# Performance work log

Measured on AMD Instinct MI355X. Metric: run time of the kernel, lower is better.

Reference implementation:

```python
import jax, jax.numpy as jnp
import numpy as np

C = 64
N_H = 4
N_WIN = 16
WIN_L = 8   # compressor window length (overlapped)
WIN_S = 4   # compressor stride -> T//4 blocks


def _rms(x, eps=1e-6):
    return x * jax.lax.rsqrt(jnp.mean(x * x, axis=-1, keepdims=True) + eps)


def _rope(x, negate=False):
    # x: (..., L, D); rotate-half RoPE over positions 0..L-1
    L, D = x.shape[-2], x.shape[-1]
    half = D // 2
    inv_freq = 1.0 / (10000.0 ** (jnp.arange(half, dtype=x.dtype) / half))
    ang = jnp.arange(L, dtype=x.dtype)[:, None] * inv_freq  # (L, half)
    if negate:
        ang = -ang
    cos, sin = jnp.cos(ang), jnp.sin(ang)
    x1, x2 = x[..., :half], x[..., half:]
    return jnp.concatenate([x1 * cos - x2 * sin, x1 * sin + x2 * cos], axis=-1)


def _compress(H, W):
    # overlapped token compressor: windows of WIN_L, stride WIN_S, zero-pad tail
    B, T, d = H.shape
    Tc = T // WIN_S
    Hp = jnp.pad(H, ((0, 0), (0, WIN_L - WIN_S), (0, 0)))
    idx = WIN_S * jnp.arange(Tc)[:, None] + jnp.arange(WIN_L)[None, :]  # (Tc, WIN_L)
    win = Hp[:, idx]                       # (B, Tc, WIN_L, d)
    return win.reshape(B, Tc, WIN_L * d) @ W  # (B, Tc, out)


def setup_inputs() -> dict:
    key = jax.random.key(0)
    ks = jax.random.split(key, 11)
    B, T, d = 2, 2048, 256

    def w(k, shape, fan):
        return jax.random.normal(k, shape, jnp.float32) / np.float32(np.sqrt(fan))

    H = jax.random.normal(ks[0], (B, T, d), jnp.float32)
    return {
        'H': H,
        'Wc_comp': w(ks[1], (WIN_L * d, C), WIN_L * d),
        'Wc_idx': w(ks[2], (WIN_L * d, 32), WIN_L * d),
        'W_DQ': w(ks[3], (d, 64), d),
        'W_IUQ': w(ks[4], (64, 4 * 32), 64),
        'W_w': w(ks[5], (64, 4), 64),
        'W_Q': w(ks[6], (d, N_H * C), d),
        'W_KV': w(ks[7], (d, C), d),
        'g_q': jnp.ones((N_H, C), jnp.float32),
        'g_k': jnp.ones((C,), jnp.float32),
        'g_v': jnp.ones((C,), jnp.float32),
        'Wg0': w(ks[8], (2 * C, 64), 2 * C),
        'bg0': jnp.zeros((64,), jnp.float32),
        'Wg1': w(ks[9], (2 * C, 64), 2 * C),
        'bg1': jnp.zeros((64,), jnp.float32),
        'Wout': w(ks[10], (128, d), 128),
        'bout': jnp.zeros((d,), jnp.float32),
    }


def reference(H, Wc_comp, Wc_idx, W_DQ, W_IUQ, W_w, W_Q, W_KV,
              g_q, g_k, g_v, Wg0, bg0, Wg1, bg1, Wout, bout):
    B, T, d = H.shape
    Tc = T // 4
    k_top = min(8, Tc)

    # ---- lightning indexer ----
    H_dc = H @ W_DQ                                   # (B,T,64)
    Q_I = (H_dc @ W_IUQ).reshape(B, T, 4, 32)         # (B,T,4,32)
    W_Iw = (H_dc @ W_w)[..., None]                    # (B,T,4,1)
    K_I = _compress(H, Wc_idx)                        # (B,Tc,32)
    dot = jnp.einsum('bthc,bsc->bths', Q_I, K_I)      # (B,T,4,Tc)
    I_ts = (W_Iw * jax.nn.relu(dot)).sum(axis=2)      # (B,T,Tc)

    t = jnp.arange(T)[:, None]
    s = jnp.arange(Tc)[None, :]
    mask_I = jnp.where(4 * s <= t, 0.0, -jnp.inf)     # (T,Tc) causal over blocks
    _, topk_idx = jax.lax.top_k(I_ts + mask_I, k_top)  # (B,T,k)
    bI = jnp.arange(B)[:, None, None]
    tI = jnp.arange(T)[None, :, None]
    M_comp = jnp.full((B, T, Tc), -jnp.inf).at[bI, tI, topk_idx].set(0.0)

    # ---- compressed + sliding KV ----
    KV = jnp.concatenate([_compress(H, Wc_comp), H @ W_KV], axis=1)  # (B,Tc+T,C)

    Q = (H @ W_Q).reshape(B, T, N_H, C).transpose(0, 2, 1, 3)        # (B,nh,T,C)
    Q = _rms(Q) * g_q[None, :, None, :]
    K = _rms(KV) * g_k
    V = _rms(KV) * g_v
    Q = _rope(Q)
    K = _rope(K)
    V = _rope(V)

    S = jnp.einsum('bhtc,bsc->bhts', Q, K) / np.float32(np.sqrt(C))  # (B,nh,T,Tc+T)

    S_comp = S[..., :Tc] + M_comp[:, None]
    rel = t - jnp.arange(T)[None, :]
    mask_slide = jnp.where((rel >= 0) & (rel < N_WIN), 0.0, -jnp.inf)  # (T,T)
    S_slide = S[..., Tc:] + mask_slide

    P = jax.nn.softmax(jnp.concatenate([S_comp, S_slide], axis=-1), axis=-1)
    O = jnp.einsum('bhts,bsc->bhtc', P, V)            # (B,nh,T,C)
    O = _rope(O, negate=True)

    O0 = O[:, :2].transpose(0, 2, 1, 3).reshape(B, T, 2 * C)
    O1 = O[:, 2:].transpose(0, 2, 1, 3).reshape(B, T, 2 * C)
    p_all = jnp.concatenate([O0 @ Wg0 + bg0, O1 @ Wg1 + bg1], axis=-1)
    return p_all @ Wout + bout
```

## Files before the change

kernel.cpp:

```cpp
#include <hip/hip_runtime.h>
#include <hip/hip_bf16.h>
#include <math.h>

#define T_DIM 2048
#define B_DIM 2
#define D_DIM 256
#define TC 512
#define KV_LEN 2560

typedef __attribute__((ext_vector_type(8))) short bf16x8;
typedef __attribute__((ext_vector_type(4))) float f32x4;
typedef unsigned short ush;

__device__ __forceinline__ float wave_sum64(float v) {
#pragma unroll
    for (int off = 32; off > 0; off >>= 1) v += __shfl_xor(v, off, 64);
    return v;
}

__device__ __forceinline__ float rope_angle(int pos, int j) {
    float inv = powf(10000.0f, -(float)j * (1.0f / 32.0f));
    return (float)pos * inv;
}

__global__ __launch_bounds__(256) void k_prep(
    const float* __restrict__ H, const float* __restrict__ W_Q,
    const float* __restrict__ W_KV, const float* __restrict__ W_DQ,
    const float* __restrict__ Wc_comp, const float* __restrict__ Wc_idx,
    ush* __restrict__ Ap, ush* __restrict__ Ac,
    ush* __restrict__ Bp, ush* __restrict__ Bc)
{
    int gid = blockIdx.x * 256 + threadIdx.x;
    float vals[8];
    ush* dst;
    bool lo_part;

    if (gid < 262144) {
        int tile = gid >> 10;
        int c = (gid >> 6) & 15;
        int l = gid & 63;
        int bt = tile * 16 + (l & 15);
        int kb = (c & 7) * 32 + (l >> 4) * 8;
        const float* src = H + (size_t)bt * 256 + kb;
#pragma unroll
        for (int j = 0; j < 8; ++j) vals[j] = src[j];
        lo_part = (c >= 8);
        dst = Ap + (size_t)gid * 8;
    } else if (gid < 786432) {
        int g = gid - 262144;
        int tile = g >> 13;
        int c = (g >> 6) & 127;
        int l = g & 63;
        int m = tile * 16 + (l & 15);
        int s = m & 511;
        int b = m >> 9;
        int k2b = (c & 63) * 32 + (l >> 4) * 8;
        int r4 = 4 * s + (k2b >> 8);
        int col = k2b & 255;
        if (r4 < T_DIM) {
            const float* src = H + ((size_t)b * T_DIM + r4) * 256 + col;
#pragma unroll
            for (int j = 0; j < 8; ++j) vals[j] = src[j];
        } else {
#pragma unroll
            for (int j = 0; j < 8; ++j) vals[j] = 0.f;
        }
        lo_part = (c >= 64);
        dst = Ac + (size_t)g * 8;
    } else if (gid < 811008) {
        int g = gid - 786432;
        int tile = g >> 10;
        int c = (g >> 6) & 15;
        int l = g & 63;
        int n = tile * 16 + (l & 15);
        int kb = (c & 7) * 32 + (l >> 4) * 8;
#pragma unroll
        for (int j = 0; j < 8; ++j) {
            int k = kb + j;
            float w;
            if (n < 256)      w = W_Q[(size_t)k * 256 + n];
            else if (n < 320) w = W_KV[(size_t)k * 64 + (n - 256)];
            else              w = W_DQ[(size_t)k * 64 + (n - 320)];
            vals[j] = w;
        }
        lo_part = (c >= 8);
        dst = Bp + (size_t)g * 8;
    } else if (gid < 860160) {
        int g = gid - 811008;
        int tile = g >> 13;
        int c = (g >> 6) & 127;
        int l = g & 63;
        int n = tile * 16 + (l & 15);
        int k2b = (c & 63) * 32 + (l >> 4) * 8;
#pragma unroll
        for (int j = 0; j < 8; ++j) {
            int k = k2b + j;
            vals[j] = (n < 64) ? Wc_comp[(size_t)k * 64 + n]
                               : Wc_idx[(size_t)k * 32 + (n - 64)];
        }
        lo_part = (c >= 64);
        dst = Bc + (size_t)g * 8;
    } else {
        return;
    }

    bf16x8 out;
#pragma unroll
    for (int j = 0; j < 8; ++j) {
        float x = vals[j];
        __hip_bfloat16 hb = __float2bfloat16(x);
        if (!lo_part) {
            out[j] = *(short*)&hb;
        } else {
            float hif = __bfloat162float(hb);
            __hip_bfloat16 lb = __float2bfloat16(x - hif);
            out[j] = *(short*)&lb;
        }
    }
    *(bf16x8*)dst = out;
}

__global__ __launch_bounds__(64) void k_mfma(
    const ush* __restrict__ Ap, const ush* __restrict__ Ac,
    const ush* __restrict__ Bp, const ush* __restrict__ Bc,
    float* __restrict__ Pre, float* __restrict__ Prec_part)
{
    int lane = threadIdx.x;
    int mrow = lane & 15;
    int q = lane >> 4;

    f32x4 acc[2][6];
#pragma unroll
    for (int mt = 0; mt < 2; ++mt)
#pragma unroll
        for (int nt = 0; nt < 6; ++nt) acc[mt][nt] = (f32x4){0.f, 0.f, 0.f, 0.f};

    if (blockIdx.x < 512) {
        int p = blockIdx.x;
        int m0 = (p >> 2) * 32;
        int n0 = (p & 3) * 96;
        int at0 = (m0 >> 4) * 16;
        int bt0n = (n0 >> 4) * 16;

        for (int c = 0; c < 8; ++c) {
            bf16x8 ahi[2], alo[2], bhi[6], blo[6];
#pragma unroll
            for (int mt = 0; mt < 2; ++mt) {
                ahi[mt] = *(const bf16x8*)(Ap + (size_t)((at0 + mt * 16) + c) * 512 + lane * 8);
                alo[mt] = *(const bf16x8*)(Ap + (size_t)((at0 + mt * 16) + 8 + c) * 512 + lane * 8);
            }
#pragma unroll
            for (int nt = 0; nt < 6; ++nt) {
                bhi[nt] = *(const bf16x8*)(Bp + (size_t)((bt0n + nt * 16) + c) * 512 + lane * 8);
                blo[nt] = *(const bf16x8*)(Bp + (size_t)((bt0n + nt * 16) + 8 + c) * 512 + lane * 8);
            }
#pragma unroll
            for (int mt = 0; mt < 2; ++mt)
#pragma unroll
                for (int nt = 0; nt < 6; ++nt) {
                    acc[mt][nt] = __builtin_amdgcn_mfma_f32_16x16x32_bf16(ahi[mt], bhi[nt], acc[mt][nt], 0, 0, 0);
                    acc[mt][nt] = __builtin_amdgcn_mfma_f32_16x16x32_bf16(ahi[mt], blo[nt], acc[mt][nt], 0, 0, 0);
                    acc[mt][nt] = __builtin_amdgcn_mfma_f32_16x16x32_bf16(alo[mt], bhi[nt], acc[mt][nt], 0, 0, 0);
                }
        }

#pragma unroll
        for (int mt = 0; mt < 2; ++mt)
#pragma unroll
            for (int nt = 0; nt < 6; ++nt)
#pragma unroll
                for (int reg = 0; reg < 4; ++reg)
                    Pre[(size_t)(m0 + 16 * mt + 4 * q + reg) * 384 + n0 + 16 * nt + mrow] =
                        acc[mt][nt][reg];
    } else {
        int cb = blockIdx.x - 512;
        int m0 = (cb >> 2) * 32;
        int q4 = cb & 3;
        int at0 = (m0 >> 4) * 128;

        for (int cl = 0; cl < 16; ++cl) {
            int c = q4 * 16 + cl;
            bf16x8 ahi[2], alo[2], bhi[6], blo[6];
#pragma unroll
            for (int mt = 0; mt < 2; ++mt) {
                ahi[mt] = *(const bf16x8*)(Ac + (size_t)((at0 + mt * 128) + c) * 512 + lane * 8);
                alo[mt] = *(const bf16x8*)(Ac + (size_t)((at0 + mt * 128) + 64 + c) * 512 + lane * 8);
            }
#pragma unroll
            for (int nt = 0; nt < 6; ++nt) {
                bhi[nt] = *(const bf16x8*)(Bc + (size_t)(nt * 128 + c) * 512 + lane * 8);
                blo[nt] = *(const bf16x8*)(Bc + (size_t)(nt * 128 + 64 + c) * 512 + lane * 8);
            }
#pragma unroll
            for (int mt = 0; mt < 2; ++mt)
#pragma unroll
                for (int nt = 0; nt < 6; ++nt) {
                    acc[mt][nt] = __builtin_amdgcn_mfma_f32_16x16x32_bf16(ahi[mt], bhi[nt], acc[mt][nt], 0, 0, 0);
                    acc[mt][nt] = __builtin_amdgcn_mfma_f32_16x16x32_bf16(ahi[mt], blo[nt], acc[mt][nt], 0, 0, 0);
                    acc[mt][nt] = __builtin_amdgcn_mfma_f32_16x16x32_bf16(alo[mt], bhi[nt], acc[mt][nt], 0, 0, 0);
                }
        }

        float* dst = Prec_part + (size_t)q4 * (1024 * 96);
#pragma unroll
        for (int mt = 0; mt < 2; ++mt)
#pragma unroll
            for (int nt = 0; nt < 6; ++nt)
#pragma unroll
                for (int reg = 0; reg < 4; ++reg)
                    dst[(size_t)(m0 + 16 * mt + 4 * q + reg) * 96 + 16 * nt + mrow] =
                        acc[mt][nt][reg];
    }
}

__global__ __launch_bounds__(256) void k_epi_proj(
    const float* __restrict__ Pre, const float* __restrict__ W_IUQ,
    const float* __restrict__ W_w, const float* __restrict__ g_q,
    const float* __restrict__ g_k, const float* __restrict__ g_v,
    float* __restrict__ QI, float* __restrict__ Wiw, float* __restrict__ Qr,
    float* __restrict__ Kbuf, float* __restrict__ Vbuf)
{
    int tid = threadIdx.x;
    int wv = tid >> 6;
    int lane = tid & 63;
    int bt = blockIdx.x * 4 + wv;
    int b = bt >> 11;
    int t = bt & 2047;

    __shared__ float sWI[8192];
    __shared__ float sWw[256];
    __shared__ float sHdc[4][64];

    for (int i = tid * 4; i < 8192; i += 1024)
        *(float4*)&sWI[i] = *(const float4*)(W_IUQ + i);
    if (tid < 64) ((float4*)sWw)[tid] = ((const float4*)W_w)[tid];

    const float* pr = Pre + (size_t)bt * 384;
    sHdc[wv][lane] = pr[320 + lane];
    __syncthreads();

    int j = lane & 31;
    float s_t, c_t;
    sincosf(rope_angle(t, j), &s_t, &c_t);

#pragma unroll
    for (int r = 0; r < 4; ++r) {
        float qv = pr[r * 64 + lane];
        float ss = wave_sum64(qv * qv);
        float sc = rsqrtf(ss * (1.0f / 64.0f) + 1e-6f);
        float qq = qv * sc * g_q[r * 64 + lane];
        float prt = __shfl_xor(qq, 32, 64);
        float o = (lane < 32) ? fmaf(qq, c_t, -prt * s_t)
                              : fmaf(prt, s_t, qq * c_t);
        Qr[(size_t)bt * 256 + r * 64 + lane] = o;
    }
    {
        float kvv = pr[256 + lane];
        float ss = wave_sum64(kvv * kvv);
        float sc = rsqrtf(ss * (1.0f / 64.0f) + 1e-6f);
        float kk = kvv * sc * g_k[lane];
        float vv = kvv * sc * g_v[lane];
        int pos = TC + t;
        float s_p, c_p;
        sincosf(rope_angle(pos, j), &s_p, &c_p);
        float pk = __shfl_xor(kk, 32, 64);
        float pv = __shfl_xor(vv, 32, 64);
        float ko = (lane < 32) ? fmaf(kk, c_p, -pk * s_p) : fmaf(pk, s_p, kk * c_p);
        float vo = (lane < 32) ? fmaf(vv, c_p, -pv * s_p) : fmaf(pv, s_p, vv * c_p);
        size_t off = ((size_t)b * KV_LEN + pos) * 64 + lane;
        Kbuf[off] = ko;
        Vbuf[off] = vo;
    }
    {
        float a0 = 0.f, a1 = 0.f;
#pragma unroll 8
        for (int jj = 0; jj < 64; ++jj) {
            float hv = sHdc[wv][jj];
            a0 = fmaf(hv, sWI[jj * 128 + lane], a0);
            a1 = fmaf(hv, sWI[jj * 128 + 64 + lane], a1);
        }
        QI[(size_t)bt * 128 + lane] = a0;
        QI[(size_t)bt * 128 + 64 + lane] = a1;
        if (lane < 4) {
            float aw = 0.f;
            for (int jj = 0; jj < 64; ++jj)
                aw = fmaf(sHdc[wv][jj], sWw[jj * 4 + lane], aw);
            Wiw[(size_t)bt * 4 + lane] = aw;
        }
    }
}

__global__ __launch_bounds__(256) void k_epi_comp(
    const float* __restrict__ Prec_part, const float* __restrict__ g_k,
    const float* __restrict__ g_v,
    float* __restrict__ KIbuf, float* __restrict__ Kbuf, float* __restrict__ Vbuf)
{
    int tid = threadIdx.x;
    int wv = tid >> 6;
    int lane = tid & 63;
    int sg = blockIdx.x * 4 + wv;
    int b = sg >> 9;
    int s = sg & 511;

    const float* p0 = Prec_part + (size_t)sg * 96;
    float kvv = p0[lane] + p0[98304 + lane] + p0[2 * 98304 + lane] + p0[3 * 98304 + lane];

    float ss = wave_sum64(kvv * kvv);
    float sc = rsqrtf(ss * (1.0f / 64.0f) + 1e-6f);
    float kk = kvv * sc * g_k[lane];
    float vv = kvv * sc * g_v[lane];
    int j = lane & 31;
    float sa, ca;
    sincosf(rope_angle(s, j), &sa, &ca);
    float pk = __shfl_xor(kk, 32, 64);
    float pv = __shfl_xor(vv, 32, 64);
    float ko = (lane < 32) ? fmaf(kk, ca, -pk * sa) : fmaf(pk, sa, kk * ca);
    float vo = (lane < 32) ? fmaf(vv, ca, -pv * sa) : fmaf(pv, sa, vv * ca);
    size_t off = ((size_t)b * KV_LEN + s) * 64 + lane;
    Kbuf[off] = ko;
    Vbuf[off] = vo;

    if (lane < 32) {
        float a = p0[64 + lane] + p0[98304 + 64 + lane] +
                  p0[2 * 98304 + 64 + lane] + p0[3 * 98304 + 64 + lane];
        KIbuf[((size_t)b * TC + s) * 32 + lane] = a;
    }
}

__global__ __launch_bounds__(256) void k_score_topk(
    const float* __restrict__ QI, const float* __restrict__ Wiw,
    const float* __restrict__ KIbuf, int* __restrict__ topk)
{
    int tid = threadIdx.x;
    int wv = tid >> 6;
    int lane = tid & 63;
    int bt0 = blockIdx.x * 4;
    int bt = bt0 + wv;
    int b = bt >> 11;
    int t = bt & 2047;

    __shared__ float sQ[4][128];
    __shared__ float sw[4][4];
    __shared__ float sKI[64 * 33];

    sQ[wv][lane] = QI[(size_t)bt * 128 + lane];
    sQ[wv][64 + lane] = QI[(size_t)bt * 128 + 64 + lane];
    if (lane < 4) sw[wv][lane] = Wiw[(size_t)bt * 4 + lane];

    const float* KIb = KIbuf + (size_t)b * TC * 32;
    int smax = t >> 2;
    int smax_blk = ((bt0 + 3) & 2047) >> 2;

    float vals[8];
#pragma unroll
    for (int r = 0; r < 8; ++r) vals[r] = -INFINITY;

    for (int r = 0; r < 8; ++r) {
        if (r * 64 > smax_blk) break;
        __syncthreads();
        for (int i = tid; i < 512; i += 256) {
            int row = i >> 3;
            int cseg = (i & 7) * 4;
            float4 v = *(const float4*)(KIb + (size_t)(r * 64 + row) * 32 + cseg);
            float* dst = &sKI[row * 33 + cseg];
            dst[0] = v.x; dst[1] = v.y; dst[2] = v.z; dst[3] = v.w;
        }
        __syncthreads();

        int s = r * 64 + lane;
        if (s <= smax) {
            float dd0 = 0.f, dd1 = 0.f, dd2 = 0.f, dd3 = 0.f;
#pragma unroll
            for (int c = 0; c < 32; ++c) {
                float kv = sKI[lane * 33 + c];
                dd0 = fmaf(sQ[wv][c], kv, dd0);
                dd1 = fmaf(sQ[wv][32 + c], kv, dd1);
                dd2 = fmaf(sQ[wv][64 + c], kv, dd2);
                dd3 = fmaf(sQ[wv][96 + c], kv, dd3);
            }
            vals[r] = sw[wv][0] * fmaxf(dd0, 0.f) + sw[wv][1] * fmaxf(dd1, 0.f) +
                      sw[wv][2] * fmaxf(dd2, 0.f) + sw[wv][3] * fmaxf(dd3, 0.f);
        }
    }

    unsigned consumed = 0u;
    for (int k2 = 0; k2 < 8; ++k2) {
        float bv = -INFINITY;
        int bi = 0x7fffffff;
#pragma unroll
        for (int r = 0; r < 8; ++r) {
            if (!(consumed & (1u << r))) {
                int s = lane + 64 * r;
                float v = vals[r];
                if (v > bv || (v == bv && s < bi)) { bv = v; bi = s; }
            }
        }
#pragma unroll
        for (int off = 1; off < 64; off <<= 1) {
            float ov = __shfl_xor(bv, off, 64);
            int oi = __shfl_xor(bi, off, 64);
            if (ov > bv || (ov == bv && oi < bi)) { bv = ov; bi = oi; }
        }
        if ((bi & 63) == lane) consumed |= 1u << (bi >> 6);
        if (lane == 0) topk[(size_t)bt * 8 + k2] = bi;
    }
}

__global__ __launch_bounds__(1024) void k_attn_out(
    const float* __restrict__ Qr, const float* __restrict__ Kbuf,
    const float* __restrict__ Vbuf, const int* __restrict__ topk,
    const float* __restrict__ Wg0, const float* __restrict__ bg0,
    const float* __restrict__ Wg1, const float* __restrict__ bg1,
    const float* __restrict__ Wout, const float* __restrict__ bout,
    float* __restrict__ out)
{
    int tid = threadIdx.x;
    int lt = tid >> 8;
    int t256 = tid & 255;
    int h = t256 >> 6;
    int lane = tid & 63;
    int bt = blockIdx.x * 4 + lt;
    int b = bt >> 11;
    int t = bt & 2047;

    __shared__ float sKV[4][48 * 65];
    __shared__ float sQ[4][256];
    __shared__ int sPos[4][24];
    __shared__ float sP[4][4][24];
    __shared__ float sO[4][256];
    __shared__ float sPall[4][128];

    sQ[lt][t256] = Qr[(size_t)bt * 256 + t256];
    if (t256 < 8) {
        sPos[lt][t256] = topk[(size_t)bt * 8 + t256];
    } else if (t256 < 24) {
        int rel = t256 - 8;
        int sp = t - rel;
        sPos[lt][t256] = (sp >= 0) ? (TC + sp) : -1;
    }
    __syncthreads();

    for (int i = t256; i < 768; i += 256) {
        int row = i >> 4;
        int seg = (i & 15) << 2;
        int key = (row < 24) ? row : row - 24;
        int pos = sPos[lt][key];
        if (pos >= 0) {
            const float* src = ((row < 24) ? Kbuf : Vbuf) +
                               ((size_t)b * KV_LEN + pos) * 64 + seg;
            float4 v = *(const float4*)src;
            float* dst = &sKV[lt][row * 65 + seg];
            dst[0] = v.x; dst[1] = v.y; dst[2] = v.z; dst[3] = v.w;
        }
    }
    __syncthreads();

    float scv = -INFINITY;
    if (lane < 24) {
        int pos = sPos[lt][lane];
        if (pos >= 0) {
            float dd = 0.f;
#pragma unroll
            for (int c = 0; c < 64; ++c)
                dd = fmaf(sQ[lt][h * 64 + c], sKV[lt][lane * 65 + c], dd);
            scv = dd * 0.125f;
        }
    }
    float m = scv;
#pragma unroll
    for (int off = 1; off < 64; off <<= 1) m = fmaxf(m, __shfl_xor(m, off, 64));
    float p = expf(scv - m);
    if (scv == -INFINITY) p = 0.f;
    float l = p;
#pragma unroll
    for (int off = 1; off < 64; off <<= 1) l += __shfl_xor(l, off, 64);
    p /= l;
    if (lane < 24) sP[lt][h][lane] = p;

    float o = 0.f;
#pragma unroll
    for (int j2 = 0; j2 < 24; ++j2) {
        int pos = sPos[lt][j2];
        if (pos >= 0)
            o = fmaf(sP[lt][h][j2], sKV[lt][(24 + j2) * 65 + lane], o);
    }

    int j = lane & 31;
    float sa, ca;
    sincosf(rope_angle(t, j), &sa, &ca);
    float prt = __shfl_xor(o, 32, 64);
    float oo = (lane < 32) ? fmaf(o, ca, prt * sa) : fmaf(-prt, sa, o * ca);
    sO[lt][h * 64 + lane] = oo;
    __syncthreads();

    if (t256 < 128) {
        float a;
        if (t256 < 64) {
            a = bg0[t256];
            for (int c = 0; c < 128; ++c) a = fmaf(sO[lt][c], Wg0[c * 64 + t256], a);
        } else {
            int i = t256 - 64;
            a = bg1[i];
            for (int c = 0; c < 128; ++c) a = fmaf(sO[lt][128 + c], Wg1[c * 64 + i], a);
        }
        sPall[lt][t256] = a;
    }
    __syncthreads();

    float a = bout[t256];
    for (int i = 0; i < 128; ++i) a = fmaf(sPall[lt][i], Wout[i * 256 + t256], a);
    out[(size_t)bt * 256 + t256] = a;
}

extern "C" void kernel_launch(void* const* d_in, const int* in_sizes, int n_in,
                              void* d_out, int out_size, void* d_ws, size_t ws_size,
                              hipStream_t stream) {
    const float* H       = (const float*)d_in[0];
    const float* Wc_comp = (const float*)d_in[1];
    const float* Wc_idx  = (const float*)d_in[2];
    const float* W_DQ    = (const float*)d_in[3];
    const float* W_IUQ   = (const float*)d_in[4];
    const float* W_w     = (const float*)d_in[5];
    const float* W_Q     = (const float*)d_in[6];
    const float* W_KV    = (const float*)d_in[7];
    const float* g_q     = (const float*)d_in[8];
    const float* g_k     = (const float*)d_in[9];
    const float* g_v     = (const float*)d_in[10];
    const float* Wg0     = (const float*)d_in[11];
    const float* bg0     = (const float*)d_in[12];
    const float* Wg1     = (const float*)d_in[13];
    const float* bg1     = (const float*)d_in[14];
    const float* Wout    = (const float*)d_in[15];
    const float* bout    = (const float*)d_in[16];

    float* ws  = (float*)d_ws;
    float* QI   = ws;
    float* Qr   = ws + 524288;
    float* Wiw  = ws + 1572864;
    float* KI   = ws + 1589248;
    float* Kb   = ws + 1622016;
    float* Vb   = ws + 1949696;
    int*   topkb = (int*)(ws + 2277376);
    float* Pre  = ws + 2310144;
    float* Prec = ws + 3883008;
    ush* Ap = (ush*)(ws + 4276224);
    ush* Ac = (ush*)(ws + 5324800);
    ush* Bp = (ush*)(ws + 7421952);
    ush* Bc = (ush*)(ws + 7520256);

    float* outp = (float*)d_out;

    hipLaunchKernelGGL(k_prep, dim3(3360), dim3(256), 0, stream,
                       H, W_Q, W_KV, W_DQ, Wc_comp, Wc_idx, Ap, Ac, Bp, Bc);
    hipLaunchKernelGGL(k_mfma, dim3(640), dim3(64), 0, stream,
                       Ap, Ac, Bp, Bc, Pre, Prec);
    hipLaunchKernelGGL(k_epi_proj, dim3(1024), dim3(256), 0, stream,
                       Pre, W_IUQ, W_w, g_q, g_k, g_v, QI, Wiw, Qr, Kb, Vb);
    hipLaunchKernelGGL(k_epi_comp, dim3(256), dim3(256), 0, stream,
                       Prec, g_k, g_v, KI, Kb, Vb);
    hipLaunchKernelGGL(k_score_topk, dim3((B_DIM * T_DIM) / 4), dim3(256), 0, stream,
                       QI, Wiw, KI, topkb);
    hipLaunchKernelGGL(k_attn_out, dim3((B_DIM * T_DIM) / 4), dim3(1024), 0, stream,
                       Qr, Kb, Vb, topkb, Wg0, bg0, Wg1, bg1, Wout, bout, outp);
}
```

Before: 193.1 us.

## Fold gate and output projections into one weight and run via MFMA

Precomputes the combined weight Wg·Wout and a combined bias in the prep kernel, stored as split-bf16 hi/lo MFMA tiles. The per-token scalar FMA loops over Wg0/Wg1/Wout at the end of attention are replaced by a separate MFMA GEMM kernel, fed by a conversion kernel that writes the attention output as split-bf16. The two epilogue kernels are also merged into one launch. This adds an Obuf round trip through global memory and two extra launches, and changes rounding slightly through the folded weights.

New measurement: 182.5 us. -5.5%, faster.

```diff
diff --git a/kernel.cpp b/kernel.cpp
--- a/kernel.cpp
+++ b/kernel.cpp
@@ -27,8 +27,12 @@
     const float* __restrict__ H, const float* __restrict__ W_Q,
     const float* __restrict__ W_KV, const float* __restrict__ W_DQ,
     const float* __restrict__ Wc_comp, const float* __restrict__ Wc_idx,
+    const float* __restrict__ Wg0, const float* __restrict__ bg0,
+    const float* __restrict__ Wg1, const float* __restrict__ bg1,
+    const float* __restrict__ Wout, const float* __restrict__ bout,
     ush* __restrict__ Ap, ush* __restrict__ Ac,
-    ush* __restrict__ Bp, ush* __restrict__ Bc)
+    ush* __restrict__ Bp, ush* __restrict__ Bc,
+    ush* __restrict__ Bo, float* __restrict__ biascomb)
 {
     int gid = blockIdx.x * 256 + threadIdx.x;
     float vals[8];
@@ -100,24 +104,55 @@
         }
         lo_part = (c >= 64);
         dst = Bc + (size_t)g * 8;
+    } else if (gid < 925696) {
+        int g = gid - 860160;
+        int k = g >> 8;
+        int n = g & 255;
+        float acc = 0.f;
+        if (k < 128) {
+            for (int i = 0; i < 64; ++i)
+                acc = fmaf(Wg0[k * 64 + i], Wout[(size_t)i * 256 + n], acc);
+        } else {
+            for (int i = 0; i < 64; ++i)
+                acc = fmaf(Wg1[(k - 128) * 64 + i], Wout[(size_t)(64 + i) * 256 + n], acc);
+        }
+        __hip_bfloat16 hb = __float2bfloat16(acc);
+        float hif = __bfloat162float(hb);
+        __hip_bfloat16 lb = __float2bfloat16(acc - hif);
+        int tile = n >> 4;
+        int chi = k >> 5;
+        int lane2 = (n & 15) + 16 * ((k >> 3) & 3);
+        int j = k & 7;
+        Bo[(size_t)(tile * 16 + chi) * 512 + lane2 * 8 + j] = *(ush*)&hb;
+        Bo[(size_t)(tile * 16 + chi + 8) * 512 + lane2 * 8 + j] = *(ush*)&lb;
+        return;
+    } else if (gid < 925952) {
+        int n = gid - 925696;
+        float acc = bout[n];
+        for (int i = 0; i < 64; ++i) {
+            acc = fmaf(bg0[i], Wout[(size_t)i * 256 + n], acc);
+            acc = fmaf(bg1[i], Wout[(size_t)(64 + i) * 256 + n], acc);
+        }
+        biascomb[n] = acc;
+        return;
     } else {
         return;
     }
 
-    bf16x8 out;
+    bf16x8 out8;
 #pragma unroll
     for (int j = 0; j < 8; ++j) {
         float x = vals[j];
         __hip_bfloat16 hb = __float2bfloat16(x);
         if (!lo_part) {
-            out[j] = *(short*)&hb;
+            out8[j] = *(short*)&hb;
         } else {
             float hif = __bfloat162float(hb);
             __hip_bfloat16 lb = __float2bfloat16(x - hif);
-            out[j] = *(short*)&lb;
-        }
-    }
-    *(bf16x8*)dst = out;
+            out8[j] = *(short*)&lb;
+        }
+    }
+    *(bf16x8*)dst = out8;
 }
 
 __global__ __launch_bounds__(64) void k_mfma(
@@ -213,117 +248,112 @@
     }
 }
 
-__global__ __launch_bounds__(256) void k_epi_proj(
-    const float* __restrict__ Pre, const float* __restrict__ W_IUQ,
-    const float* __restrict__ W_w, const float* __restrict__ g_q,
-    const float* __restrict__ g_k, const float* __restrict__ g_v,
+__global__ __launch_bounds__(256) void k_epi(
+    const float* __restrict__ Pre, const float* __restrict__ Prec_part,
+    const float* __restrict__ W_IUQ, const float* __restrict__ W_w,
+    const float* __restrict__ g_q, const float* __restrict__ g_k,
+    const float* __restrict__ g_v,
     float* __restrict__ QI, float* __restrict__ Wiw, float* __restrict__ Qr,
-    float* __restrict__ Kbuf, float* __restrict__ Vbuf)
+    float* __restrict__ KIbuf, float* __restrict__ Kbuf, float* __restrict__ Vbuf)
 {
+    __shared__ float sWI[8192];
+    __shared__ float sWw[256];
+    __shared__ float sHdc[4][64];
+
     int tid = threadIdx.x;
     int wv = tid >> 6;
     int lane = tid & 63;
-    int bt = blockIdx.x * 4 + wv;
-    int b = bt >> 11;
-    int t = bt & 2047;
-
-    __shared__ float sWI[8192];
-    __shared__ float sWw[256];
-    __shared__ float sHdc[4][64];
-
-    for (int i = tid * 4; i < 8192; i += 1024)
-        *(float4*)&sWI[i] = *(const float4*)(W_IUQ + i);
-    if (tid < 64) ((float4*)sWw)[tid] = ((const float4*)W_w)[tid];
-
-    const float* pr = Pre + (size_t)bt * 384;
-    sHdc[wv][lane] = pr[320 + lane];
-    __syncthreads();
-
-    int j = lane & 31;
-    float s_t, c_t;
-    sincosf(rope_angle(t, j), &s_t, &c_t);
-
-#pragma unroll
-    for (int r = 0; r < 4; ++r) {
-        float qv = pr[r * 64 + lane];
-        float ss = wave_sum64(qv * qv);
-        float sc = rsqrtf(ss * (1.0f / 64.0f) + 1e-6f);
-        float qq = qv * sc * g_q[r * 64 + lane];
-        float prt = __shfl_xor(qq, 32, 64);
-        float o = (lane < 32) ? fmaf(qq, c_t, -prt * s_t)
-                              : fmaf(prt, s_t, qq * c_t);
-        Qr[(size_t)bt * 256 + r * 64 + lane] = o;
-    }
-    {
-        float kvv = pr[256 + lane];
+
+    if (blockIdx.x < 1024) {
+        int bt = blockIdx.x * 4 + wv;
+        int b = bt >> 11;
+        int t = bt & 2047;
+
+        for (int i = tid * 4; i < 8192; i += 1024)
+            *(float4*)&sWI[i] = *(const float4*)(W_IUQ + i);
+        if (tid < 64) ((float4*)sWw)[tid] = ((const float4*)W_w)[tid];
+
+        const float* pr = Pre + (size_t)bt * 384;
+        sHdc[wv][lane] = pr[320 + lane];
+        __syncthreads();
+
+        int j = lane & 31;
+        float s_t, c_t;
+        sincosf(rope_angle(t, j), &s_t, &c_t);
+
+#pragma unroll
+        for (int r = 0; r < 4; ++r) {
+            float qv = pr[r * 64 + lane];
+            float ss = wave_sum64(qv * qv);
+            float sc = rsqrtf(ss * (1.0f / 64.0f) + 1e-6f);
+            float qq = qv * sc * g_q[r * 64 + lane];
+            float prt = __shfl_xor(qq, 32, 64);
+            float o = (lane < 32) ? fmaf(qq, c_t, -prt * s_t)
+                                  : fmaf(prt, s_t, qq * c_t);
+            Qr[(size_t)bt * 256 + r * 64 + lane] = o;
+        }
+        {
+            float kvv = pr[256 + lane];
+            float ss = wave_sum64(kvv * kvv);
+            float sc = rsqrtf(ss * (1.0f / 64.0f) + 1e-6f);
+            float kk = kvv * sc * g_k[lane];
+            float vv = kvv * sc * g_v[lane];
+            int pos = TC + t;
+            float s_p, c_p;
+            sincosf(rope_angle(pos, j), &s_p, &c_p);
+            float pk = __shfl_xor(kk, 32, 64);
+            float pv = __shfl_xor(vv, 32, 64);
+            float ko = (lane < 32) ? fmaf(kk, c_p, -pk * s_p) : fmaf(pk, s_p, kk * c_p);
+            float vo = (lane < 32) ? fmaf(vv, c_p, -pv * s_p) : fmaf(pv, s_p, vv * c_p);
+            size_t off = ((size_t)b * KV_LEN + pos) * 64 + lane;
+            Kbuf[off] = ko;
+            Vbuf[off] = vo;
+        }
+        {
+            float a0 = 0.f, a1 = 0.f;
+#pragma unroll 8
+            for (int jj = 0; jj < 64; ++jj) {
+                float hv = sHdc[wv][jj];
+                a0 = fmaf(hv, sWI[jj * 128 + lane], a0);
+                a1 = fmaf(hv, sWI[jj * 128 + 64 + lane], a1);
+            }
+            QI[(size_t)bt * 128 + lane] = a0;
+            QI[(size_t)bt * 128 + 64 + lane] = a1;
+            if (lane < 4) {
+                float aw = 0.f;
+                for (int jj = 0; jj < 64; ++jj)
+                    aw = fmaf(sHdc[wv][jj], sWw[jj * 4 + lane], aw);
+                Wiw[(size_t)bt * 4 + lane] = aw;
+            }
+        }
+    } else {
+        int sg = (blockIdx.x - 1024) * 4 + wv;
+        int b = sg >> 9;
+        int s = sg & 511;
+
+        const float* p0 = Prec_part + (size_t)sg * 96;
+        float kvv = p0[lane] + p0[98304 + lane] + p0[2 * 98304 + lane] + p0[3 * 98304 + lane];
+
         float ss = wave_sum64(kvv * kvv);
         float sc = rsqrtf(ss * (1.0f / 64.0f) + 1e-6f);
         float kk = kvv * sc * g_k[lane];
         float vv = kvv * sc * g_v[lane];
-        int pos = TC + t;
-        float s_p, c_p;
-        sincosf(rope_angle(pos, j), &s_p, &c_p);
+        int j = lane & 31;
+        float sa, ca;
+        sincosf(rope_angle(s, j), &sa, &ca);
         float pk = __shfl_xor(kk, 32, 64);
         float pv = __shfl_xor(vv, 32, 64);
-        float ko = (lane < 32) ? fmaf(kk, c_p, -pk * s_p) : fmaf(pk, s_p, kk * c_p);
-        float vo = (lane < 32) ? fmaf(vv, c_p, -pv * s_p) : fmaf(pv, s_p, vv * c_p);
-        size_t off = ((size_t)b * KV_LEN + pos) * 64 + lane;
+        float ko = (lane < 32) ? fmaf(kk, ca, -pk * sa) : fmaf(pk, sa, kk * ca);
+        float vo = (lane < 32) ? fmaf(vv, ca, -pv * sa) : fmaf(pv, sa, vv * ca);
+        size_t off = ((size_t)b * KV_LEN + s) * 64 + lane;
         Kbuf[off] = ko;
         Vbuf[off] = vo;
-    }
-    {
-        float a0 = 0.f, a1 = 0.f;
-#pragma unroll 8
-        for (int jj = 0; jj < 64; ++jj) {
-            float hv = sHdc[wv][jj];
-            a0 = fmaf(hv, sWI[jj * 128 + lane], a0);
-            a1 = fmaf(hv, sWI[jj * 128 + 64 + lane], a1);
-        }
-        QI[(size_t)bt * 128 + lane] = a0;
-        QI[(size_t)bt * 128 + 64 + lane] = a1;
-        if (lane < 4) {
-            float aw = 0.f;
-            for (int jj = 0; jj < 64; ++jj)
-                aw = fmaf(sHdc[wv][jj], sWw[jj * 4 + lane], aw);
-            Wiw[(size_t)bt * 4 + lane] = aw;
-        }
-    }
-}
-
-__global__ __launch_bounds__(256) void k_epi_comp(
-    const float* __restrict__ Prec_part, const float* __restrict__ g_k,
-    const float* __restrict__ g_v,
-    float* __restrict__ KIbuf, float* __restrict__ Kbuf, float* __restrict__ Vbuf)
-{
-    int tid = threadIdx.x;
-    int wv = tid >> 6;
-    int lane = tid & 63;
-    int sg = blockIdx.x * 4 + wv;
-    int b = sg >> 9;
-    int s = sg & 511;
-
-    const float* p0 = Prec_part + (size_t)sg * 96;
-    float kvv = p0[lane] + p0[98304 + lane] + p0[2 * 98304 + lane] + p0[3 * 98304 + lane];
-
-    float ss = wave_sum64(kvv * kvv);
-    float sc = rsqrtf(ss * (1.0f / 64.0f) + 1e-6f);
-    float kk = kvv * sc * g_k[lane];
-    float vv = kvv * sc * g_v[lane];
-    int j = lane & 31;
-    float sa, ca;
-    sincosf(rope_angle(s, j), &sa, &ca);
-    float pk = __shfl_xor(kk, 32, 64);
-    float pv = __shfl_xor(vv, 32, 64);
-    float ko = (lane < 32) ? fmaf(kk, ca, -pk * sa) : fmaf(pk, sa, kk * ca);
-    float vo = (lane < 32) ? fmaf(vv, ca, -pv * sa) : fmaf(pv, sa, vv * ca);
-    size_t off = ((size_t)b * KV_LEN + s) * 64 + lane;
-    Kbuf[off] = ko;
-    Vbuf[off] = vo;
-
-    if (lane < 32) {
-        float a = p0[64 + lane] + p0[98304 + 64 + lane] +
-                  p0[2 * 98304 + 64 + lane] + p0[3 * 98304 + 64 + lane];
-        KIbuf[((size_t)b * TC + s) * 32 + lane] = a;
+
+        if (lane < 32) {
+            float a = p0[64 + lane] + p0[98304 + 64 + lane] +
+                      p0[2 * 98304 + 64 + lane] + p0[3 * 98304 + 64 + lane];
+            KIbuf[((size_t)b * TC + s) * 32 + lane] = a;
+        }
     }
 }
 
@@ -406,13 +436,10 @@
     }
 }
 
-__global__ __launch_bounds__(1024) void k_attn_out(
+__global__ __launch_bounds__(1024) void k_attn(
     const float* __restrict__ Qr, const float* __restrict__ Kbuf,
     const float* __restrict__ Vbuf, const int* __restrict__ topk,
-    const float* __restrict__ Wg0, const float* __restrict__ bg0,
-    const float* __restrict__ Wg1, const float* __restrict__ bg1,
-    const float* __restrict__ Wout, const float* __restrict__ bout,
-    float* __restrict__ out)
+    float* __restrict__ Obuf)
 {
     int tid = threadIdx.x;
     int lt = tid >> 8;
@@ -427,8 +454,6 @@
     __shared__ float sQ[4][256];
     __shared__ int sPos[4][24];
     __shared__ float sP[4][4][24];
-    __shared__ float sO[4][256];
-    __shared__ float sPall[4][128];
 
     sQ[lt][t256] = Qr[(size_t)bt * 256 + t256];
     if (t256 < 8) {
@@ -490,26 +515,87 @@
     sincosf(rope_angle(t, j), &sa, &ca);
     float prt = __shfl_xor(o, 32, 64);
     float oo = (lane < 32) ? fmaf(o, ca, prt * sa) : fmaf(-prt, sa, o * ca);
-    sO[lt][h * 64 + lane] = oo;
-    __syncthreads();
-
-    if (t256 < 128) {
-        float a;
-        if (t256 < 64) {
-            a = bg0[t256];
-            for (int c = 0; c < 128; ++c) a = fmaf(sO[lt][c], Wg0[c * 64 + t256], a);
+    Obuf[(size_t)bt * 256 + h * 64 + lane] = oo;
+}
+
+__global__ __launch_bounds__(256) void k_cvtO(
+    const float* __restrict__ Obuf, ush* __restrict__ Ao)
+{
+    int gid = blockIdx.x * 256 + threadIdx.x;
+    int tile = gid >> 10;
+    int c = (gid >> 6) & 15;
+    int l = gid & 63;
+    int row = tile * 16 + (l & 15);
+    int kb = (c & 7) * 32 + (l >> 4) * 8;
+    const float* src = Obuf + (size_t)row * 256 + kb;
+    bool lo_part = (c >= 8);
+    bf16x8 out8;
+#pragma unroll
+    for (int j = 0; j < 8; ++j) {
+        float x = src[j];
+        __hip_bfloat16 hb = __float2bfloat16(x);
+        if (!lo_part) {
+            out8[j] = *(short*)&hb;
         } else {
-            int i = t256 - 64;
-            a = bg1[i];
-            for (int c = 0; c < 128; ++c) a = fmaf(sO[lt][128 + c], Wg1[c * 64 + i], a);
-        }
-        sPall[lt][t256] = a;
-    }
-    __syncthreads();
-
-    float a = bout[t256];
-    for (int i = 0; i < 128; ++i) a = fmaf(sPall[lt][i], Wout[i * 256 + t256], a);
-    out[(size_t)bt * 256 + t256] = a;
+            float hif = __bfloat162float(hb);
+            __hip_bfloat16 lb = __float2bfloat16(x - hif);
+            out8[j] = *(short*)&lb;
+        }
+    }
+    *(bf16x8*)(Ao + (size_t)gid * 8) = out8;
+}
+
+__global__ __launch_bounds__(64) void k_out(
+    const ush* __restrict__ Ao, const ush* __restrict__ Bo,
+    const float* __restrict__ biascomb, float* __restrict__ out)
+{
+    int lane = threadIdx.x;
+    int mrow = lane & 15;
+    int q = lane >> 4;
+    int p = blockIdx.x;
+    int m0 = (p >> 2) * 32;
+    int n0 = (p & 3) * 64;
+    int at0 = (m0 >> 4) * 16;
+    int bt0n = (n0 >> 4) * 16;
+
+    f32x4 acc[2][4];
+#pragma unroll
+    for (int mt = 0; mt < 2; ++mt)
+#pragma unroll
+        for (int nt = 0; nt < 4; ++nt) acc[mt][nt] = (f32x4){0.f, 0.f, 0.f, 0.f};
+
+    for (int c = 0; c < 8; ++c) {
+        bf16x8 ahi[2], alo[2], bhi[4], blo[4];
+#pragma unroll
+        for (int mt = 0; mt < 2; ++mt) {
+            ahi[mt] = *(const bf16x8*)(Ao + (size_t)((at0 + mt * 16) + c) * 512 + lane * 8);
+            alo[mt] = *(const bf16x8*)(Ao + (size_t)((at0 + mt * 16) + 8 + c) * 512 + lane * 8);
+        }
+#pragma unroll
+        for (int nt = 0; nt < 4; ++nt) {
+            bhi[nt] = *(const bf16x8*)(Bo + (size_t)((bt0n + nt * 16) + c) * 512 + lane * 8);
+            blo[nt] = *(const bf16x8*)(Bo + (size_t)((bt0n + nt * 16) + 8 + c) * 512 + lane * 8);
+        }
+#pragma unroll
+        for (int mt = 0; mt < 2; ++mt)
+#pragma unroll
+            for (int nt = 0; nt < 4; ++nt) {
+                acc[mt][nt] = __builtin_amdgcn_mfma_f32_16x16x32_bf16(ahi[mt], bhi[nt], acc[mt][nt], 0, 0, 0);
+                acc[mt][nt] = __builtin_amdgcn_mfma_f32_16x16x32_bf16(ahi[mt], blo[nt], acc[mt][nt], 0, 0, 0);
+                acc[mt][nt] = __builtin_amdgcn_mfma_f32_16x16x32_bf16(alo[mt], bhi[nt], acc[mt][nt], 0, 0, 0);
+            }
+    }
+
+#pragma unroll
+    for (int mt = 0; mt < 2; ++mt)
+#pragma unroll
+        for (int nt = 0; nt < 4; ++nt) {
+            float bia = biascomb[n0 + 16 * nt + mrow];
+#pragma unroll
+            for (int reg = 0; reg < 4; ++reg)
+                out[(size_t)(m0 + 16 * mt + 4 * q + reg) * 256 + n0 + 16 * nt + mrow] =
+                    acc[mt][nt][reg] + bia;
+        }
 }
 
 extern "C" void kernel_launch(void* const* d_in, const int* in_sizes, int n_in,
@@ -534,32 +620,41 @@
     const float* bout    = (const float*)d_in[16];
 
     float* ws  = (float*)d_ws;
-    float* QI   = ws;
-    float* Qr   = ws + 524288;
-    float* Wiw  = ws + 1572864;
-    float* KI   = ws + 1589248;
-    float* Kb   = ws + 1622016;
-    float* Vb   = ws + 1949696;
+    float* QI    = ws;
+    float* Qr    = ws + 524288;
+    float* Wiw   = ws + 1572864;
+    float* KI    = ws + 1589248;
+    float* Kb    = ws + 1622016;
+    float* Vb    = ws + 1949696;
     int*   topkb = (int*)(ws + 2277376);
-    float* Pre  = ws + 2310144;
-    float* Prec = ws + 3883008;
+    float* Pre   = ws + 2310144;
+    float* Prec  = ws + 3883008;
     ush* Ap = (ush*)(ws + 4276224);
     ush* Ac = (ush*)(ws + 5324800);
     ush* Bp = (ush*)(ws + 7421952);
     ush* Bc = (ush*)(ws + 7520256);
+    ush* Bo = (ush*)(ws + 7716864);
+    float* biascomb = ws + 7782400;
+    float* Obuf = ws + 4276224;
+    ush*   Ao   = (ush*)(ws + 5324800);
 
     float* outp = (float*)d_out;
 
-    hipLaunchKernelGGL(k_prep, dim3(3360), dim3(256), 0, stream,
-                       H, W_Q, W_KV, W_DQ, Wc_comp, Wc_idx, Ap, Ac, Bp, Bc);
+    hipLaunchKernelGGL(k_prep, dim3(3617), dim3(256), 0, stream,
+                       H, W_Q, W_KV, W_DQ, Wc_comp, Wc_idx,
+                       Wg0, bg0, Wg1, bg1, Wout, bout,
+                       Ap, Ac, Bp, Bc, Bo, biascomb);
     hipLaunchKernelGGL(k_mfma, dim3(640), dim3(64), 0, stream,
                        Ap, Ac, Bp, Bc, Pre, Prec);
-    hipLaunchKernelGGL(k_epi_proj, dim3(1024), dim3(256), 0, stream,
-                       Pre, W_IUQ, W_w, g_q, g_k, g_v, QI, Wiw, Qr, Kb, Vb);
-    hipLaunchKernelGGL(k_epi_comp, dim3(256), dim3(256), 0, stream,
-                       Prec, g_k, g_v, KI, Kb, Vb);
+    hipLaunchKernelGGL(k_epi, dim3(1280), dim3(256), 0, stream,
+                       Pre, Prec, W_IUQ, W_w, g_q, g_k, g_v,
+                       QI, Wiw, Qr, KI, Kb, Vb);
     hipLaunchKernelGGL(k_score_topk, dim3((B_DIM * T_DIM) / 4), dim3(256), 0, stream,
                        QI, Wiw, KI, topkb);
-    hipLaunchKernelGGL(k_attn_out, dim3((B_DIM * T_DIM) / 4), dim3(1024), 0, stream,
-                       Qr, Kb, Vb, topkb, Wg0, bg0, Wg1, bg1, Wout, bout, outp);
-}
+    hipLaunchKernelGGL(k_attn, dim3((B_DIM * T_DIM) / 4), dim3(1024), 0, stream,
+                       Qr, Kb, Vb, topkb, Obuf);
+    hipLaunchKernelGGL(k_cvtO, dim3(1024), dim3(256), 0, stream,
+                       Obuf, Ao);
+    hipLaunchKernelGGL(k_out, dim3(512), dim3(64), 0, stream,
+                       Ao, Bo, biascomb, outp);
+}
```
